# Kernel tuning notes

Measured on AMD Instinct MI355X. Metric: run time of the kernel, lower is better.

## Reference

```python
import jax, jax.numpy as jnp
import numpy as np

D_MODEL = 512
H = 8
D_K = D_MODEL // H


def setup_inputs() -> dict:
    key = jax.random.key(0)
    ks = jax.random.split(key, 11)
    B, S = 2, 4096
    scale = 1.0 / np.sqrt(D_MODEL)
    inp = {
        "q": jax.random.normal(ks[0], (B, S, D_MODEL), jnp.float32),
        "k": jax.random.normal(ks[1], (B, S, D_MODEL), jnp.float32),
        "v": jax.random.normal(ks[2], (B, S, D_MODEL), jnp.float32),
        "wq": jax.random.normal(ks[3], (D_MODEL, D_MODEL), jnp.float32) * scale,
        "bq": jnp.zeros((D_MODEL,), jnp.float32),
        "wk": jax.random.normal(ks[4], (D_MODEL, D_MODEL), jnp.float32) * scale,
        "bk": jnp.zeros((D_MODEL,), jnp.float32),
        "wv": jax.random.normal(ks[5], (D_MODEL, D_MODEL), jnp.float32) * scale,
        "bv": jnp.zeros((D_MODEL,), jnp.float32),
        "wo": jax.random.normal(ks[6], (D_MODEL, D_MODEL), jnp.float32) * scale,
        "bo": jnp.zeros((D_MODEL,), jnp.float32),
    }
    return inp


def reference(q, k, v, wq, bq, wk, bk, wv, bv, wo, bo):
    B, S, _ = q.shape
    # Linear projections (torch Linear: x @ W.T + b), split into heads -> [B,H,S,Dk]
    def proj(x, w, b):
        y = jnp.einsum('bsd,ed->bse', x, w) + b
        return y.reshape(B, -1, H, D_K).transpose(0, 2, 1, 3)

    qh = proj(q, wq, bq)
    kh = proj(k, wk, bk)
    vh = proj(v, wv, bv)

    # scaled dot-product attention, full [B,H,S,S] scores (faithful to source)
    scores = jnp.einsum('bhqd,bhkd->bhqk', qh, kh) / jnp.sqrt(jnp.asarray(D_K, qh.dtype))
    attn = jax.nn.softmax(scores, axis=-1)
    x = jnp.einsum('bhqk,bhkd->bhqd', attn, vh)

    # merge heads and output projection
    x = x.transpose(0, 2, 1, 3).reshape(B, S, H * D_K)
    return jnp.einsum('bsd,ed->bse', x, wo) + bo
```

## Files before the change

kernel.cpp:

```cpp
#include <hip/hip_runtime.h>

#define DM 512
#define NH 8
#define DK 64
#define SEQ 4096

typedef short bf16x8 __attribute__((ext_vector_type(8)));
typedef float f32x4 __attribute__((ext_vector_type(4)));
typedef unsigned short u16;
typedef u16 u16x8 __attribute__((ext_vector_type(8)));
typedef u16 u16x4 __attribute__((ext_vector_type(4)));
typedef unsigned int u32;
typedef u32 u32x2 __attribute__((ext_vector_type(2)));

__device__ __forceinline__ u16 f2bf(float f) {
  union { float f; unsigned u; } v; v.f = f;
  unsigned r = v.u + 0x7fffu + ((v.u >> 16) & 1u);
  return (u16)(r >> 16);
}

__device__ __forceinline__ u32 cvtpk(float a, float b) {
  u32 r; asm("v_cvt_pk_bf16_f32 %0, %1, %2" : "=v"(r) : "v"(a), "v"(b)); return r;
}

__device__ __forceinline__ float fexp2(float x) {
  float r; asm("v_exp_f32 %0, %1" : "=v"(r) : "v"(x)); return r;
}

__device__ __forceinline__ float fmax3(float a, float b, float c) {
  return fmaxf(fmaxf(a, b), c);
}

__global__ __launch_bounds__(256, 2)
void gemm_qkv(const float* __restrict__ qx, const float* __restrict__ kx,
              const float* __restrict__ vx,
              const float* __restrict__ wq, const float* __restrict__ bq,
              const float* __restrict__ wk, const float* __restrict__ bk,
              const float* __restrict__ wv, const float* __restrict__ bv,
              u16* __restrict__ Qh, u16* __restrict__ Kh, u16* __restrict__ Vt)
{
  __shared__ alignas(16) u16 Alds[64][72];
  __shared__ alignas(16) u16 Blds[128][72];
  const int mode = blockIdx.x >> 9;
  const int bid = blockIdx.x & 511;
  const float* X = (mode == 0) ? qx : (mode == 1) ? kx : vx;
  const float* W = (mode == 0) ? wq : (mode == 1) ? wk : wv;
  const float* Bs = (mode == 0) ? bq : (mode == 1) ? bk : bv;

  const int t = threadIdx.x;
  const int bx = bid & 127, by = bid >> 7;
  const int m0 = bx << 6, n0 = by << 7;
  const int lane = t & 63, w = t >> 6;
  const int lr = lane & 15, lg = lane >> 4;
  const int wr = w >> 1, wc = w & 1;

  f32x4 acc[2][4];
  #pragma unroll
  for (int i = 0; i < 2; ++i)
    #pragma unroll
    for (int j = 0; j < 4; ++j) acc[i][j] = (f32x4){0.f, 0.f, 0.f, 0.f};

  float4 xa[4]; float4 wb[8];
  auto loadX = [&](int k0) {
    #pragma unroll
    for (int i = 0; i < 4; ++i) {
      int f = (i << 8) + t;
      xa[i] = *(const float4*)(X + (size_t)(m0 + (f >> 4)) * 512 + k0 + ((f & 15) << 2));
    }
    #pragma unroll
    for (int i = 0; i < 8; ++i) {
      int f = (i << 8) + t;
      wb[i] = *(const float4*)(W + (size_t)(n0 + (f >> 4)) * 512 + k0 + ((f & 15) << 2));
    }
  };

  loadX(0);
  for (int k0 = 0; k0 < 512; k0 += 64) {
    __syncthreads();
    #pragma unroll
    for (int i = 0; i < 4; ++i) {
      int f = (i << 8) + t;
      u16x4 p = { f2bf(xa[i].x), f2bf(xa[i].y), f2bf(xa[i].z), f2bf(xa[i].w) };
      *(u16x4*)&Alds[f >> 4][(f & 15) << 2] = p;
    }
    #pragma unroll
    for (int i = 0; i < 8; ++i) {
      int f = (i << 8) + t;
      u16x4 p = { f2bf(wb[i].x), f2bf(wb[i].y), f2bf(wb[i].z), f2bf(wb[i].w) };
      *(u16x4*)&Blds[f >> 4][(f & 15) << 2] = p;
    }
    __syncthreads();
    if (k0 + 64 < 512) loadX(k0 + 64);

    #pragma unroll
    for (int kk = 0; kk < 2; ++kk) {
      bf16x8 af[2], bfr[4];
      #pragma unroll
      for (int mi = 0; mi < 2; ++mi)
        af[mi] = *(const bf16x8*)&Alds[(wr << 5) + (mi << 4) + lr][(kk << 5) + (lg << 3)];
      #pragma unroll
      for (int ni = 0; ni < 4; ++ni)
        bfr[ni] = *(const bf16x8*)&Blds[(wc << 6) + (ni << 4) + lr][(kk << 5) + (lg << 3)];
      #pragma unroll
      for (int mi = 0; mi < 2; ++mi)
        #pragma unroll
        for (int ni = 0; ni < 4; ++ni)
          acc[mi][ni] = __builtin_amdgcn_mfma_f32_16x16x32_bf16(af[mi], bfr[ni], acc[mi][ni], 0, 0, 0);
    }
  }

  const float sc = (mode == 0) ? 0.18033688f : 1.0f;
  #pragma unroll
  for (int mi = 0; mi < 2; ++mi) {
    #pragma unroll
    for (int ni = 0; ni < 4; ++ni) {
      const int e = n0 + (wc << 6) + (ni << 4) + lr;
      const int m = m0 + (wr << 5) + (mi << 4) + (lg << 2);
      const float bb = Bs[e];
      const int b = m >> 12, s = m & 4095, h = e >> 6, dk = e & 63;
      if (mode != 2) {
        u16* O = (mode == 0) ? Qh : Kh;
        size_t base = ((size_t)((b << 3) + h) * SEQ + s) * DK + dk;
        #pragma unroll
        for (int r = 0; r < 4; ++r)
          O[base + (size_t)r * DK] = f2bf((acc[mi][ni][r] + bb) * sc);
      } else {
        size_t base = ((size_t)((b << 3) + h) * DK + dk) * SEQ + s;
        u16x4 p = { f2bf(acc[mi][ni][0] + bb), f2bf(acc[mi][ni][1] + bb),
                    f2bf(acc[mi][ni][2] + bb), f2bf(acc[mi][ni][3] + bb) };
        *(u16x4*)(Vt + base) = p;
      }
    }
  }
}

__global__ __launch_bounds__(256, 2)
void gemm_out(const u16* __restrict__ Xa, const float* __restrict__ W,
              const float* __restrict__ bias, float* __restrict__ Out)
{
  __shared__ alignas(16) u16 Alds[64][72];
  __shared__ alignas(16) u16 Blds[128][72];
  const int t = threadIdx.x;
  const int bx = blockIdx.x & 127, by = blockIdx.x >> 7;
  const int m0 = bx << 6, n0 = by << 7;
  const int lane = t & 63, w = t >> 6;
  const int lr = lane & 15, lg = lane >> 4;
  const int wr = w >> 1, wc = w & 1;

  f32x4 acc[2][4];
  #pragma unroll
  for (int i = 0; i < 2; ++i)
    #pragma unroll
    for (int j = 0; j < 4; ++j) acc[i][j] = (f32x4){0.f, 0.f, 0.f, 0.f};

  u16x8 xa3[2]; float4 wb[8];
  auto loadX = [&](int k0) {
    #pragma unroll
    for (int i = 0; i < 2; ++i) {
      int f = (i << 8) + t;
      xa3[i] = *(const u16x8*)(Xa + (size_t)(m0 + (f >> 3)) * 512 + k0 + ((f & 7) << 3));
    }
    #pragma unroll
    for (int i = 0; i < 8; ++i) {
      int f = (i << 8) + t;
      wb[i] = *(const float4*)(W + (size_t)(n0 + (f >> 4)) * 512 + k0 + ((f & 15) << 2));
    }
  };

  loadX(0);
  for (int k0 = 0; k0 < 512; k0 += 64) {
    __syncthreads();
    #pragma unroll
    for (int i = 0; i < 2; ++i) {
      int f = (i << 8) + t;
      *(u16x8*)&Alds[f >> 3][(f & 7) << 3] = xa3[i];
    }
    #pragma unroll
    for (int i = 0; i < 8; ++i) {
      int f = (i << 8) + t;
      u16x4 p = { f2bf(wb[i].x), f2bf(wb[i].y), f2bf(wb[i].z), f2bf(wb[i].w) };
      *(u16x4*)&Blds[f >> 4][(f & 15) << 2] = p;
    }
    __syncthreads();
    if (k0 + 64 < 512) loadX(k0 + 64);

    #pragma unroll
    for (int kk = 0; kk < 2; ++kk) {
      bf16x8 af[2], bfr[4];
      #pragma unroll
      for (int mi = 0; mi < 2; ++mi)
        af[mi] = *(const bf16x8*)&Alds[(wr << 5) + (mi << 4) + lr][(kk << 5) + (lg << 3)];
      #pragma unroll
      for (int ni = 0; ni < 4; ++ni)
        bfr[ni] = *(const bf16x8*)&Blds[(wc << 6) + (ni << 4) + lr][(kk << 5) + (lg << 3)];
      #pragma unroll
      for (int mi = 0; mi < 2; ++mi)
        #pragma unroll
        for (int ni = 0; ni < 4; ++ni)
          acc[mi][ni] = __builtin_amdgcn_mfma_f32_16x16x32_bf16(af[mi], bfr[ni], acc[mi][ni], 0, 0, 0);
    }
  }

  #pragma unroll
  for (int mi = 0; mi < 2; ++mi) {
    #pragma unroll
    for (int ni = 0; ni < 4; ++ni) {
      const int e = n0 + (wc << 6) + (ni << 4) + lr;
      const int m = m0 + (wr << 5) + (mi << 4) + (lg << 2);
      const float bb = bias[e];
      size_t base = (size_t)m * 512 + e;
      #pragma unroll
      for (int r = 0; r < 4; ++r) Out[base + (size_t)r * 512] = acc[mi][ni][r] + bb;
    }
  }
}

__global__ __launch_bounds__(256, 2)
void attn_kernel(const u16* __restrict__ Qh, const u16* __restrict__ Kh,
                 const u16* __restrict__ Vt, u16* __restrict__ Xa)
{
  __shared__ alignas(16) u16 smem[12800];

  const int t = threadIdx.x;
  const int lane = t & 63, w = t >> 6;
  const int lr = lane & 15, lg = lane >> 4;
  const int ob = ((blockIdx.x & 7) << 6) + (blockIdx.x >> 3);
  const int qb = ob & 31, bh = ob >> 5;
  const size_t qkbase = (size_t)bh * SEQ * DK;
  const size_t vbase  = (size_t)bh * DK * SEQ;
  u16* Pw = smem + 8192 + w * 1152;

  bf16x8 qf[2][2];
  #pragma unroll
  for (int mi = 0; mi < 2; ++mi)
    #pragma unroll
    for (int kk = 0; kk < 2; ++kk) {
      int qrow = (qb << 7) + (w << 5) + (mi << 4) + lr;
      qf[mi][kk] = *(const bf16x8*)(Qh + qkbase + (size_t)qrow * DK + (kk << 5) + (lg << 3));
    }

  bf16x8 onesf;
  {
    u16 one = (lr == 0) ? (u16)0x3F80 : (u16)0;
    #pragma unroll
    for (int j = 0; j < 8; ++j) onesf[j] = (short)one;
  }

  float mrun[2] = {0.f, 0.f};
  f32x4 o[2][4], osum[2];
  #pragma unroll
  for (int mi = 0; mi < 2; ++mi) {
    #pragma unroll
    for (int dt = 0; dt < 4; ++dt) o[mi][dt] = (f32x4){0.f, 0.f, 0.f, 0.f};
    osum[mi] = (f32x4){0.f, 0.f, 0.f, 0.f};
  }

  const u16* Kg = Kh + qkbase;
  const u16* Vg = Vt + vbase;
  const int r0 = t >> 3, c0 = t & 7;
  const int r1 = r0 + 32, c1 = c0;
  const int wk0 = r0 * 64 + ((c0 ^ (r0 & 7)) << 3);
  const int wk1 = r1 * 64 + ((c1 ^ (r1 & 7)) << 3);

  u16x8 kr0, kr1, vr0, vr1;
  kr0 = *(const u16x8*)(Kg + (size_t)r0 * 64 + (c0 << 3));
  kr1 = *(const u16x8*)(Kg + (size_t)r1 * 64 + (c1 << 3));
  vr0 = *(const u16x8*)(Vg + (size_t)r0 * SEQ + (c0 << 3));
  vr1 = *(const u16x8*)(Vg + (size_t)r1 * SEQ + (c1 << 3));

  for (int it = 0; it < SEQ / 64; ++it) {
    __syncthreads();
    *(u16x8*)&smem[wk0]        = kr0;
    *(u16x8*)&smem[wk1]        = kr1;
    *(u16x8*)&smem[4096 + wk0] = vr0;
    *(u16x8*)&smem[4096 + wk1] = vr1;
    __syncthreads();
    if (it + 1 < SEQ / 64) {
      const int kv0n = (it + 1) << 6;
      kr0 = *(const u16x8*)(Kg + (size_t)(kv0n + r0) * 64 + (c0 << 3));
      kr1 = *(const u16x8*)(Kg + (size_t)(kv0n + r1) * 64 + (c1 << 3));
      vr0 = *(const u16x8*)(Vg + (size_t)r0 * SEQ + kv0n + (c0 << 3));
      vr1 = *(const u16x8*)(Vg + (size_t)r1 * SEQ + kv0n + (c1 << 3));
    }

    bf16x8 kf[4][2], vf[4][2];
    #pragma unroll
    for (int nt = 0; nt < 4; ++nt)
      #pragma unroll
      for (int kk = 0; kk < 2; ++kk) {
        const int off = ((nt << 4) + lr) * 64 + ((((kk << 2) + lg) ^ (lr & 7)) << 3);
        kf[nt][kk] = *(const bf16x8*)&smem[off];
        vf[nt][kk] = *(const bf16x8*)&smem[4096 + off];
      }

    #pragma unroll
    for (int mi = 0; mi < 2; ++mi) {
      f32x4 s[4];
      #pragma unroll
      for (int nt = 0; nt < 4; ++nt) s[nt] = (f32x4){0.f, 0.f, 0.f, 0.f};
      __builtin_amdgcn_s_setprio(1);
      #pragma unroll
      for (int kk = 0; kk < 2; ++kk)
        #pragma unroll
        for (int nt = 0; nt < 4; ++nt)
          s[nt] = __builtin_amdgcn_mfma_f32_16x16x32_bf16(kf[nt][kk], qf[mi][kk], s[nt], 0, 0, 0);
      __builtin_amdgcn_s_setprio(0);

      float m0 = fmax3(s[0][0], s[0][1], s[0][2]);
      float m1 = fmax3(s[0][3], s[1][0], s[1][1]);
      float m2 = fmax3(s[1][2], s[1][3], s[2][0]);
      float m3 = fmax3(s[2][1], s[2][2], s[2][3]);
      float m4 = fmax3(s[3][0], s[3][1], s[3][2]);
      float tmax = fmaxf(fmax3(m0, m1, m2), fmax3(m3, m4, s[3][3]));
      tmax = fmaxf(tmax, __shfl_xor(tmax, 16));
      tmax = fmaxf(tmax, __shfl_xor(tmax, 32));

      const float mm = mrun[mi];
      #pragma unroll
      for (int nt = 0; nt < 4; ++nt) {
        s[nt][0] = fexp2(s[nt][0] - mm);
        s[nt][1] = fexp2(s[nt][1] - mm);
        s[nt][2] = fexp2(s[nt][2] - mm);
        s[nt][3] = fexp2(s[nt][3] - mm);
      }

      if (!__all(tmax <= mm + 8.f)) {
        float mnew = fmaxf(mm, tmax);
        float f = fexp2(mm - mnew);
        mrun[mi] = mnew;
        osum[mi][0] *= f;
        #pragma unroll
        for (int dt = 0; dt < 4; ++dt) o[mi][dt] *= f;
        #pragma unroll
        for (int nt = 0; nt < 4; ++nt) s[nt] *= f;
      }

      #pragma unroll
      for (int nt = 0; nt < 4; ++nt) {
        u32x2 pk2 = { cvtpk(s[nt][0], s[nt][1]), cvtpk(s[nt][2], s[nt][3]) };
        *(u32x2*)((char*)Pw + lr * 144 + (nt << 5) + (lg << 3)) = pk2;
      }

      #pragma unroll
      for (int kk = 0; kk < 2; ++kk) {
        bf16x8 pf = *(const bf16x8*)&Pw[lr * 72 + (kk << 5) + (lg << 3)];
        __builtin_amdgcn_s_setprio(1);
        #pragma unroll
        for (int dt = 0; dt < 4; ++dt)
          o[mi][dt] = __builtin_amdgcn_mfma_f32_16x16x32_bf16(vf[dt][kk], pf, o[mi][dt], 0, 0, 0);
        osum[mi] = __builtin_amdgcn_mfma_f32_16x16x32_bf16(onesf, pf, osum[mi], 0, 0, 0);
        __builtin_amdgcn_s_setprio(0);
      }
    }
  }
  __syncthreads();

  #pragma unroll
  for (int mi = 0; mi < 2; ++mi) {
    float lsum = __shfl(osum[mi][0], lr);
    float inv = 1.f / lsum;
    #pragma unroll
    for (int dt = 0; dt < 4; ++dt) {
      u16x4 v4 = { f2bf(o[mi][dt][0] * inv), f2bf(o[mi][dt][1] * inv),
                   f2bf(o[mi][dt][2] * inv), f2bf(o[mi][dt][3] * inv) };
      int row = (w << 5) + (mi << 4) + lr;
      *(u16x4*)&smem[row * 72 + (dt << 4) + (lg << 2)] = v4;
    }
  }
  __syncthreads();
  {
    const int b = bh >> 3, h = bh & 7;
    #pragma unroll
    for (int i = 0; i < 4; ++i) {
      int f = (i << 8) + t;
      int row = f >> 3, c8 = (f & 7) << 3;
      u16x8 val = *(const u16x8*)&smem[row * 72 + c8];
      *(u16x8*)(Xa + ((size_t)b * SEQ + (qb << 7) + row) * DM + (h << 6) + c8) = val;
    }
  }
}

extern "C" void kernel_launch(void* const* d_in, const int* in_sizes, int n_in,
                              void* d_out, int out_size, void* d_ws, size_t ws_size,
                              hipStream_t stream)
{
  const float* q  = (const float*)d_in[0];
  const float* k  = (const float*)d_in[1];
  const float* v  = (const float*)d_in[2];
  const float* wq = (const float*)d_in[3];
  const float* bq = (const float*)d_in[4];
  const float* wk = (const float*)d_in[5];
  const float* bk = (const float*)d_in[6];
  const float* wv = (const float*)d_in[7];
  const float* bv = (const float*)d_in[8];
  const float* wo = (const float*)d_in[9];
  const float* bo = (const float*)d_in[10];

  const size_t HS = (size_t)2 * NH * SEQ * DK;
  u16* Qh = (u16*)d_ws;
  u16* Kh = Qh + HS;
  u16* Vt = Kh + HS;
  u16* Xa = Vt + HS;

  gemm_qkv<<<1536, 256, 0, stream>>>(q, k, v, wq, bq, wk, bk, wv, bv, Qh, Kh, Vt);
  attn_kernel<<<512, 256, 0, stream>>>(Qh, Kh, Vt, Xa);
  gemm_out<<<512, 256, 0, stream>>>(Xa, wo, bo, (float*)d_out);
}
```

Measured before the change: 150.9 us.

## Double-buffer K/V tiles in LDS and reorder online-softmax rescale before exp

The attention loop now uses two LDS buffers for the K/V tiles, so there is one barrier per iteration instead of two. The next tile is written to the idle buffer right after fragments are read, and global loads are issued two tiles ahead. The online-softmax max update now happens before exponentiation, so P no longer needs rescaling, and the running max starts at a large negative value. The s_setprio hints around the MFMAs are removed. LDS use rises from about 25KB to about 41KB per block, which may reduce occupancy below the two blocks per CU the launch bounds target.

```diff
diff --git a/kernel.cpp b/kernel.cpp
--- a/kernel.cpp
+++ b/kernel.cpp
@@ -219,7 +219,7 @@
 void attn_kernel(const u16* __restrict__ Qh, const u16* __restrict__ Kh,
                  const u16* __restrict__ Vt, u16* __restrict__ Xa)
 {
-  __shared__ alignas(16) u16 smem[12800];
+  __shared__ alignas(1024) u16 smem[20992];
 
   const int t = threadIdx.x;
   const int lane = t & 63, w = t >> 6;
@@ -228,7 +228,7 @@
   const int qb = ob & 31, bh = ob >> 5;
   const size_t qkbase = (size_t)bh * SEQ * DK;
   const size_t vbase  = (size_t)bh * DK * SEQ;
-  u16* Pw = smem + 8192 + w * 1152;
+  u16* Pw = smem + 16384 + w * 1152;
 
   bf16x8 qf[2][2];
   #pragma unroll
@@ -246,7 +246,7 @@
     for (int j = 0; j < 8; ++j) onesf[j] = (short)one;
   }
 
-  float mrun[2] = {0.f, 0.f};
+  float mrun[2] = {-3e38f, -3e38f};
   f32x4 o[2][4], osum[2];
   #pragma unroll
   for (int mi = 0; mi < 2; ++mi) {
@@ -258,53 +258,57 @@
   const u16* Kg = Kh + qkbase;
   const u16* Vg = Vt + vbase;
   const int r0 = t >> 3, c0 = t & 7;
-  const int r1 = r0 + 32, c1 = c0;
+  const int r1 = r0 + 32;
   const int wk0 = r0 * 64 + ((c0 ^ (r0 & 7)) << 3);
-  const int wk1 = r1 * 64 + ((c1 ^ (r1 & 7)) << 3);
+  const int wk1 = r1 * 64 + ((c0 ^ (r1 & 7)) << 3);
 
   u16x8 kr0, kr1, vr0, vr1;
-  kr0 = *(const u16x8*)(Kg + (size_t)r0 * 64 + (c0 << 3));
-  kr1 = *(const u16x8*)(Kg + (size_t)r1 * 64 + (c1 << 3));
-  vr0 = *(const u16x8*)(Vg + (size_t)r0 * SEQ + (c0 << 3));
-  vr1 = *(const u16x8*)(Vg + (size_t)r1 * SEQ + (c1 << 3));
+  auto GLOAD = [&](int it2) {
+    const int kv0 = it2 << 6;
+    kr0 = *(const u16x8*)(Kg + (size_t)(kv0 + r0) * 64 + (c0 << 3));
+    kr1 = *(const u16x8*)(Kg + (size_t)(kv0 + r1) * 64 + (c0 << 3));
+    vr0 = *(const u16x8*)(Vg + (size_t)r0 * SEQ + kv0 + (c0 << 3));
+    vr1 = *(const u16x8*)(Vg + (size_t)r1 * SEQ + kv0 + (c0 << 3));
+  };
+  auto WRITE = [&](int buf) {
+    u16* B = smem + buf * 8192;
+    *(u16x8*)&B[wk0]        = kr0;
+    *(u16x8*)&B[wk1]        = kr1;
+    *(u16x8*)&B[4096 + wk0] = vr0;
+    *(u16x8*)&B[4096 + wk1] = vr1;
+  };
+
+  GLOAD(0); WRITE(0); GLOAD(1);
 
   for (int it = 0; it < SEQ / 64; ++it) {
+    const int cur = it & 1;
     __syncthreads();
-    *(u16x8*)&smem[wk0]        = kr0;
-    *(u16x8*)&smem[wk1]        = kr1;
-    *(u16x8*)&smem[4096 + wk0] = vr0;
-    *(u16x8*)&smem[4096 + wk1] = vr1;
-    __syncthreads();
-    if (it + 1 < SEQ / 64) {
-      const int kv0n = (it + 1) << 6;
-      kr0 = *(const u16x8*)(Kg + (size_t)(kv0n + r0) * 64 + (c0 << 3));
-      kr1 = *(const u16x8*)(Kg + (size_t)(kv0n + r1) * 64 + (c1 << 3));
-      vr0 = *(const u16x8*)(Vg + (size_t)r0 * SEQ + kv0n + (c0 << 3));
-      vr1 = *(const u16x8*)(Vg + (size_t)r1 * SEQ + kv0n + (c1 << 3));
-    }
-
+
+    const u16* Kb = smem + cur * 8192;
+    const u16* Vb = Kb + 4096;
     bf16x8 kf[4][2], vf[4][2];
     #pragma unroll
     for (int nt = 0; nt < 4; ++nt)
       #pragma unroll
       for (int kk = 0; kk < 2; ++kk) {
         const int off = ((nt << 4) + lr) * 64 + ((((kk << 2) + lg) ^ (lr & 7)) << 3);
-        kf[nt][kk] = *(const bf16x8*)&smem[off];
-        vf[nt][kk] = *(const bf16x8*)&smem[4096 + off];
+        kf[nt][kk] = *(const bf16x8*)&Kb[off];
+        vf[nt][kk] = *(const bf16x8*)&Vb[off];
       }
+
+    if (it + 1 < SEQ / 64) WRITE(cur ^ 1);
+    if (it + 2 < SEQ / 64) GLOAD(it + 2);
 
     #pragma unroll
     for (int mi = 0; mi < 2; ++mi) {
       f32x4 s[4];
       #pragma unroll
       for (int nt = 0; nt < 4; ++nt) s[nt] = (f32x4){0.f, 0.f, 0.f, 0.f};
-      __builtin_amdgcn_s_setprio(1);
       #pragma unroll
       for (int kk = 0; kk < 2; ++kk)
         #pragma unroll
         for (int nt = 0; nt < 4; ++nt)
           s[nt] = __builtin_amdgcn_mfma_f32_16x16x32_bf16(kf[nt][kk], qf[mi][kk], s[nt], 0, 0, 0);
-      __builtin_amdgcn_s_setprio(0);
 
       float m0 = fmax3(s[0][0], s[0][1], s[0][2]);
       float m1 = fmax3(s[0][3], s[1][0], s[1][1]);
@@ -315,41 +319,31 @@
       tmax = fmaxf(tmax, __shfl_xor(tmax, 16));
       tmax = fmaxf(tmax, __shfl_xor(tmax, 32));
 
+      if (!__all(tmax <= mrun[mi] + 8.f)) {
+        float mnew = fmaxf(mrun[mi], tmax);
+        float scl = fexp2(mrun[mi] - mnew);
+        mrun[mi] = mnew;
+        osum[mi][0] *= scl;
+        #pragma unroll
+        for (int dt = 0; dt < 4; ++dt) o[mi][dt] *= scl;
+      }
       const float mm = mrun[mi];
+
       #pragma unroll
       for (int nt = 0; nt < 4; ++nt) {
-        s[nt][0] = fexp2(s[nt][0] - mm);
-        s[nt][1] = fexp2(s[nt][1] - mm);
-        s[nt][2] = fexp2(s[nt][2] - mm);
-        s[nt][3] = fexp2(s[nt][3] - mm);
-      }
-
-      if (!__all(tmax <= mm + 8.f)) {
-        float mnew = fmaxf(mm, tmax);
-        float f = fexp2(mm - mnew);
-        mrun[mi] = mnew;
-        osum[mi][0] *= f;
-        #pragma unroll
-        for (int dt = 0; dt < 4; ++dt) o[mi][dt] *= f;
-        #pragma unroll
-        for (int nt = 0; nt < 4; ++nt) s[nt] *= f;
-      }
-
-      #pragma unroll
-      for (int nt = 0; nt < 4; ++nt) {
-        u32x2 pk2 = { cvtpk(s[nt][0], s[nt][1]), cvtpk(s[nt][2], s[nt][3]) };
+        float e0 = fexp2(s[nt][0] - mm), e1 = fexp2(s[nt][1] - mm);
+        float e2 = fexp2(s[nt][2] - mm), e3 = fexp2(s[nt][3] - mm);
+        u32x2 pk2 = { cvtpk(e0, e1), cvtpk(e2, e3) };
         *(u32x2*)((char*)Pw + lr * 144 + (nt << 5) + (lg << 3)) = pk2;
       }
 
       #pragma unroll
       for (int kk = 0; kk < 2; ++kk) {
         bf16x8 pf = *(const bf16x8*)&Pw[lr * 72 + (kk << 5) + (lg << 3)];
-        __builtin_amdgcn_s_setprio(1);
         #pragma unroll
         for (int dt = 0; dt < 4; ++dt)
           o[mi][dt] = __builtin_amdgcn_mfma_f32_16x16x32_bf16(vf[dt][kk], pf, o[mi][dt], 0, 0, 0);
         osum[mi] = __builtin_amdgcn_mfma_f32_16x16x32_bf16(onesf, pf, osum[mi], 0, 0, 0);
-        __builtin_amdgcn_s_setprio(0);
       }
     }
   }
```

New measurement: 146.1 us. 3.2% less time.
